# Kernel tuning notes

Hardware: AMD Instinct MI355X
Metric: run time of the kernel (lower is better)

## Reference

```python
import jax, jax.numpy as jnp
import numpy as np

HIDDEN = 1024
HEADS = 16
HEAD_DIM = HIDDEN // HEADS  # 64; softmax scale uses head_dim per SeqAttention(hidden_size=head_dim)


def setup_inputs() -> dict:
    key = jax.random.key(0)
    ks = jax.random.split(key, 7)
    B, M = 2, 2048
    s = 1.0 / np.sqrt(HIDDEN)
    return {
        "query": jax.random.normal(ks[0], (B, M, HIDDEN), jnp.float32),
        "key": jax.random.normal(ks[1], (B, M, HIDDEN), jnp.float32),
        "value": jax.random.normal(ks[2], (B, M, HIDDEN), jnp.float32),
        "Wq": jax.random.normal(ks[3], (HIDDEN, HIDDEN), jnp.float32) * s,
        "Wk": jax.random.normal(ks[4], (HIDDEN, HIDDEN), jnp.float32) * s,
        "Wv": jax.random.normal(ks[5], (HIDDEN, HIDDEN), jnp.float32) * s,
        "Wo": jax.random.normal(ks[6], (HIDDEN, HIDDEN), jnp.float32) * s,
    }


def _split_heads(x):
    # [B, T, H*D] -> [B, H, T, D]
    B, T, _ = x.shape
    return x.reshape(B, T, HEADS, HEAD_DIM).transpose(0, 2, 1, 3)


def reference(query, key, value, Wq, Wk, Wv, Wo):
    # nn.Linear(bias=False): y = x @ W.T
    q = _split_heads(query @ Wq.T)  # [B,H,M,D]
    k = _split_heads(key @ Wk.T)    # [B,H,N,D]
    v = _split_heads(value @ Wv.T)  # [B,H,N,D]
    scale = 1.0 / jnp.sqrt(jnp.asarray(HEAD_DIM, q.dtype))
    attn = jnp.einsum("bhmd,bhnd->bhmn", q, k) * scale
    attn = jax.nn.softmax(attn, axis=-1)
    out = jnp.einsum("bhmn,bhnd->bhmd", attn, v)  # [B,H,M,D]
    B, H, M, D = out.shape
    out = out.transpose(0, 2, 1, 3).reshape(B, M, H * D)
    return out @ Wo.T
```

## Files before the change

kernel.cpp:

```cpp
#include <hip/hip_runtime.h>

typedef __bf16 bf16;
typedef __bf16 bf16x2 __attribute__((ext_vector_type(2)));
typedef __bf16 bf16x8 __attribute__((ext_vector_type(8)));
typedef float  f32x4  __attribute__((ext_vector_type(4)));
typedef float  f32x16 __attribute__((ext_vector_type(16)));
typedef unsigned int u32;
typedef unsigned int u32x4 __attribute__((ext_vector_type(4)));

typedef __attribute__((address_space(1))) unsigned int gu32;
typedef __attribute__((address_space(3))) unsigned int lu32;

__device__ __forceinline__ void llds16(const void* g, void* l) {
  __builtin_amdgcn_global_load_lds((gu32*)g, (lu32*)l, 16, 0, 0);
}

__device__ __forceinline__ void cvt8(const float* __restrict__ src,
                                     bf16* __restrict__ dst, int i) {
  const float4* s4 = (const float4*)src;
  float4 a = s4[i * 2 + 0];
  float4 c = s4[i * 2 + 1];
  bf16x8 o;
  o[0] = (bf16)a.x; o[1] = (bf16)a.y; o[2] = (bf16)a.z; o[3] = (bf16)a.w;
  o[4] = (bf16)c.x; o[5] = (bf16)c.y; o[6] = (bf16)c.z; o[7] = (bf16)c.w;
  ((bf16x8*)dst)[i] = o;
}

__global__ __launch_bounds__(256) void cvt_bf16(const float* __restrict__ src,
                                                bf16* __restrict__ dst, int n8) {
  int i = blockIdx.x * blockDim.x + threadIdx.x;
  if (i < n8) cvt8(src, dst, i);
}

__global__ __launch_bounds__(256) void cvt_all(const float* __restrict__ w0,
                                               const float* __restrict__ w1,
                                               const float* __restrict__ w2,
                                               const float* __restrict__ w3,
                                               const float* __restrict__ x0,
                                               const float* __restrict__ x1,
                                               const float* __restrict__ x2,
                                               bf16* __restrict__ wdst,
                                               bf16* __restrict__ xdst) {
  const int b = blockIdx.x;
  if (b < 2048) {
    const int which = b >> 9;
    const float* src = (which == 0) ? w0 : (which == 1) ? w1 : (which == 2) ? w2 : w3;
    const int i = (b & 511) * 256 + threadIdx.x;
    cvt8(src, wdst + (size_t)which * (1u << 20), i);
  } else {
    const int b2 = b - 2048;
    const int which = b2 >> 11;
    const float* src = (which == 0) ? x0 : (which == 1) ? x1 : x2;
    const int i = (b2 & 2047) * 256 + threadIdx.x;
    cvt8(src, xdst + (size_t)which * (4u << 20), i);
  }
}

__global__ __launch_bounds__(256) void gemm_qkv(const bf16* __restrict__ A0,
                                                const bf16* __restrict__ A1,
                                                const bf16* __restrict__ A2,
                                                const bf16* __restrict__ Wb,
                                                bf16* __restrict__ qb,
                                                bf16* __restrict__ kb,
                                                bf16* __restrict__ vb,
                                                int zoff) {
  constexpr int K = 1024, BM = 128, BN = 128, BK = 32, NT = K / BK;
  __shared__ bf16 Alds[2][BM * BK];
  __shared__ bf16 Blds[2][BN * BK];
  const int t = threadIdx.x, w = t >> 6, l = t & 63;
  const int lr = l & 15, lg = l >> 4;
  const int bm = blockIdx.x * BM, bn = blockIdx.y * BN;
  const int z = blockIdx.z + zoff;
  const bf16* A = (z == 0) ? A0 : (z == 1) ? A1 : A2;
  const bf16* W = Wb + (size_t)z * (1u << 20);
  const int wm = (w >> 1) * 64, wn = (w & 1) * 64;

  f32x4 acc[4][4] = {};

  auto stage = [&](int buf, int kt) {
    const int k0 = kt * BK;
#pragma unroll
    for (int i = 0; i < 2; ++i) {
      int idx = i * 256 + t;
      int row = idx >> 2, kb2 = (idx & 3) * 16;
      llds16((const char*)A + ((size_t)(bm + row) * K + k0) * 2 + kb2,
             (char*)(&Alds[buf][0]) + (i * 4 + w) * 1024);
    }
#pragma unroll
    for (int i = 0; i < 2; ++i) {
      int idx = i * 256 + t;
      int row = idx >> 2, kb2 = (idx & 3) * 16;
      llds16((const char*)W + ((size_t)(bn + row) * K + k0) * 2 + kb2,
             (char*)(&Blds[buf][0]) + (i * 4 + w) * 1024);
    }
  };

  stage(0, 0);
  for (int kt = 0; kt < NT; ++kt) {
    __syncthreads();
    if (kt + 1 < NT) stage((kt + 1) & 1, kt + 1);
    const int cur = kt & 1;
    bf16x8 af[4], bfr[4];
#pragma unroll
    for (int i = 0; i < 4; ++i)
      af[i] = *(const bf16x8*)(&Alds[cur][(wm + i * 16 + lr) * BK + lg * 8]);
#pragma unroll
    for (int j = 0; j < 4; ++j)
      bfr[j] = *(const bf16x8*)(&Blds[cur][(wn + j * 16 + lr) * BK + lg * 8]);
    __builtin_amdgcn_s_setprio(1);
#pragma unroll
    for (int i = 0; i < 4; ++i)
#pragma unroll
      for (int j = 0; j < 4; ++j)
        acc[i][j] = __builtin_amdgcn_mfma_f32_16x16x32_bf16(af[i], bfr[j], acc[i][j], 0, 0, 0);
    __builtin_amdgcn_s_setprio(0);
  }

  bf16* Cout = (z == 0) ? qb : (z == 1) ? kb : vb;
  const float osc = (z == 0) ? 0.1803368801f : 1.0f;
#pragma unroll
  for (int i = 0; i < 4; ++i) {
#pragma unroll
    for (int j = 0; j < 4; ++j) {
#pragma unroll
      for (int r = 0; r < 4; ++r) {
        const int gm = bm + wm + i * 16 + lg * 4 + r;
        const int n  = bn + wn + j * 16 + lr;
        const int b = gm >> 11, m = gm & 2047;
        const int h = n >> 6, d = n & 63;
        const size_t off = (z < 2)
            ? ((size_t)((b * 16 + h) * 2048 + m) * 64 + d)
            : ((size_t)((b * 16 + h) * 64 + d) * 2048 + m);
        Cout[off] = (bf16)(acc[i][j][r] * osc);
      }
    }
  }
}

__global__ __launch_bounds__(256) void gemm_out(const bf16* __restrict__ A,
                                                const bf16* __restrict__ Bw,
                                                float* __restrict__ Cout) {
  constexpr int N = 1024, K = 1024;
  constexpr int BM = 128, BN = 64, BK = 32;
  __shared__ bf16 Alds[2][BM * BK];
  __shared__ bf16 Blds[2][BN * BK];
  const int t = threadIdx.x;
  const int w = t >> 6, l = t & 63;
  const int lr = l & 15, lg = l >> 4;
  const int bm = blockIdx.x * BM, bn = blockIdx.y * BN;
  const int wm = (w >> 1) * 64, wn = (w & 1) * 32;

  f32x4 acc[4][2] = {};

  auto stage = [&](int buf, int kt) {
    const int k0 = kt * BK;
#pragma unroll
    for (int i = 0; i < 2; ++i) {
      int idx = i * 256 + t;
      int row = idx >> 2, kb = (idx & 3) * 16;
      const char* g = (const char*)A + ((size_t)(bm + row) * K + k0) * 2 + kb;
      llds16(g, (char*)(&Alds[buf][0]) + (i * 4 + w) * 1024);
    }
    {
      int row = t >> 2, kb = (t & 3) * 16;
      const char* g = (const char*)Bw + ((size_t)(bn + row) * K + k0) * 2 + kb;
      llds16(g, (char*)(&Blds[buf][0]) + w * 1024);
    }
  };

  stage(0, 0);
  constexpr int NT = K / BK;
  for (int kt = 0; kt < NT; ++kt) {
    __syncthreads();
    if (kt + 1 < NT) stage((kt + 1) & 1, kt + 1);
    const int cur = kt & 1;
    bf16x8 af[4], bfr[2];
#pragma unroll
    for (int i = 0; i < 4; ++i)
      af[i] = *(const bf16x8*)(&Alds[cur][(wm + i * 16 + lr) * BK + lg * 8]);
#pragma unroll
    for (int j = 0; j < 2; ++j)
      bfr[j] = *(const bf16x8*)(&Blds[cur][(wn + j * 16 + lr) * BK + lg * 8]);
    __builtin_amdgcn_s_setprio(1);
#pragma unroll
    for (int i = 0; i < 4; ++i)
#pragma unroll
      for (int j = 0; j < 2; ++j)
        acc[i][j] = __builtin_amdgcn_mfma_f32_16x16x32_bf16(af[i], bfr[j], acc[i][j], 0, 0, 0);
    __builtin_amdgcn_s_setprio(0);
  }

#pragma unroll
  for (int i = 0; i < 4; ++i)
#pragma unroll
    for (int j = 0; j < 2; ++j)
#pragma unroll
      for (int r = 0; r < 4; ++r) {
        const int gm = bm + wm + i * 16 + lg * 4 + r;
        const int n  = bn + wn + j * 16 + lr;
        Cout[(size_t)gm * N + n] = acc[i][j][r];
      }
}

__global__ __launch_bounds__(256) void attn_fwd(const bf16* __restrict__ Qb,
                                                const bf16* __restrict__ Kb,
                                                const bf16* __restrict__ Vt,
                                                bf16* __restrict__ Out) {
  constexpr int Mlen = 2048, KVB = 64, NTT = Mlen / KVB;
  __shared__ bf16 Klds[4][KVB * 64];
  __shared__ bf16 Vlds[4][64 * KVB];
  const int t = threadIdx.x, w = t >> 6, l = t & 63;
  const int l31 = l & 31, hi = l >> 5;
  const int orig = blockIdx.x;
  const int wg = (orig & 7) * 64 + (orig >> 3);
  const int bh = wg >> 4;
  const int qr = (wg & 15) * 128 + w * 32;
  const int key = (l31 & 7) << 4;

  const bf16* qbase = Qb + ((size_t)bh * Mlen + qr + l31) * 64;
  bf16x8 qf[4];
#pragma unroll
  for (int dks = 0; dks < 4; ++dks)
    qf[dks] = *(const bf16x8*)(qbase + dks * 16 + hi * 8);

  u32x4 onesw;
  onesw[0] = 0x3F803F80u; onesw[1] = 0x3F803F80u;
  onesw[2] = 0x3F803F80u; onesw[3] = 0x3F803F80u;
  const bf16x8 ones = __builtin_bit_cast(bf16x8, onesw);

  f32x16 acco0 = {}, acco1 = {};
  f32x16 accl = {};

  const char* kTile0 = (const char*)Kb + (size_t)bh * Mlen * 64 * 2;
  const char* vBase  = (const char*)Vt + (size_t)bh * 64 * Mlen * 2;

  auto stageKV = [&](int buf, int tile) {
    const int kv0 = tile * KVB;
#pragma unroll
    for (int i = 0; i < 2; ++i) {
      int idx = i * 256 + t;
      int L = idx * 16;
      int row = L >> 7;
      int inner = (L & 127) ^ ((row & 7) << 4);
      llds16(kTile0 + (size_t)(kv0 + row) * 128 + inner,
             (char*)(&Klds[buf][0]) + (i * 4 + w) * 1024);
    }
#pragma unroll
    for (int i = 0; i < 2; ++i) {
      int idx = i * 256 + t;
      int L = idx * 16;
      int d = L >> 7;
      int inner = (L & 127) ^ ((d & 7) << 4);
      llds16(vBase + (size_t)d * (Mlen * 2) + kv0 * 2 + inner,
             (char*)(&Vlds[buf][0]) + (i * 4 + w) * 1024);
    }
  };

  auto STEP_HEAD = [&](int tile) {
    if (tile + 1 < NTT) {
      stageKV((tile + 1) & 3, tile + 1);
      asm volatile("s_waitcnt vmcnt(4)" ::: "memory");
    } else {
      asm volatile("s_waitcnt vmcnt(0)" ::: "memory");
    }
    __builtin_amdgcn_s_barrier();
    __builtin_amdgcn_sched_barrier(0);
  };
  auto QK = [&](int tile, f32x16& s0, f32x16& s1) {
    const char* kb_ = (const char*)(&Klds[tile & 3][0]);
    __builtin_amdgcn_s_setprio(1);
#pragma unroll
    for (int dks = 0; dks < 4; ++dks) {
      const int a0 = (0 * 32 + l31) * 128 + ((dks * 32 + hi * 16) ^ key);
      const int a1 = (1 * 32 + l31) * 128 + ((dks * 32 + hi * 16) ^ key);
      bf16x8 kf0 = *(const bf16x8*)(kb_ + a0);
      bf16x8 kf1 = *(const bf16x8*)(kb_ + a1);
      s0 = __builtin_amdgcn_mfma_f32_32x32x16_bf16(kf0, qf[dks], s0, 0, 0, 0);
      s1 = __builtin_amdgcn_mfma_f32_32x32x16_bf16(kf1, qf[dks], s1, 0, 0, 0);
    }
    __builtin_amdgcn_s_setprio(0);
  };
  auto EXP = [&](const f32x16& s0, const f32x16& s1, u32 (&w0)[8], u32 (&w1)[8]) {
#pragma unroll
    for (int e2 = 0; e2 < 8; ++e2) {
      const float p00 = __builtin_amdgcn_exp2f(s0[2 * e2]);
      const float p01 = __builtin_amdgcn_exp2f(s0[2 * e2 + 1]);
      const float p10 = __builtin_amdgcn_exp2f(s1[2 * e2]);
      const float p11 = __builtin_amdgcn_exp2f(s1[2 * e2 + 1]);
      bf16x2 k0; k0[0] = (bf16)p00; k0[1] = (bf16)p01;
      bf16x2 k1; k1[0] = (bf16)p10; k1[1] = (bf16)p11;
      w0[e2] = __builtin_bit_cast(u32, k0);
      w1[e2] = __builtin_bit_cast(u32, k1);
    }
  };
  auto PV = [&](int tprev, const u32 (&w0)[8], const u32 (&w1)[8]) {
    const char* vb_ = (const char*)(&Vlds[tprev & 3][0]);
    __builtin_amdgcn_s_setprio(1);
#pragma unroll
    for (int ks = 0; ks < 2; ++ks) {
      auto sa0 = __builtin_amdgcn_permlane32_swap(w0[4 * ks + 0], w0[4 * ks + 2], false, false);
      auto sa1 = __builtin_amdgcn_permlane32_swap(w0[4 * ks + 1], w0[4 * ks + 3], false, false);
      auto sb0 = __builtin_amdgcn_permlane32_swap(w1[4 * ks + 0], w1[4 * ks + 2], false, false);
      auto sb1 = __builtin_amdgcn_permlane32_swap(w1[4 * ks + 1], w1[4 * ks + 3], false, false);
      u32x4 fa, fb;
      fa[0] = (u32)sa0[0]; fa[1] = (u32)sa1[0]; fa[2] = (u32)sa0[1]; fa[3] = (u32)sa1[1];
      fb[0] = (u32)sb0[0]; fb[1] = (u32)sb1[0]; fb[2] = (u32)sb0[1]; fb[3] = (u32)sb1[1];
      const bf16x8 pa = __builtin_bit_cast(bf16x8, fa);
      const bf16x8 pb = __builtin_bit_cast(bf16x8, fb);
      const int c0 = (ks * 32 + hi * 16);
      bf16x8 va0 = *(const bf16x8*)(vb_ + (0 * 32 + l31) * 128 + ((0 * 64 + c0) ^ key));
      bf16x8 va1 = *(const bf16x8*)(vb_ + (1 * 32 + l31) * 128 + ((0 * 64 + c0) ^ key));
      bf16x8 vb0 = *(const bf16x8*)(vb_ + (0 * 32 + l31) * 128 + ((1 * 64 + c0) ^ key));
      bf16x8 vb1 = *(const bf16x8*)(vb_ + (1 * 32 + l31) * 128 + ((1 * 64 + c0) ^ key));
      acco0 = __builtin_amdgcn_mfma_f32_32x32x16_bf16(pa, va0, acco0, 0, 0, 0);
      acco1 = __builtin_amdgcn_mfma_f32_32x32x16_bf16(pa, va1, acco1, 0, 0, 0);
      accl  = __builtin_amdgcn_mfma_f32_32x32x16_bf16(pa, ones, accl, 0, 0, 0);
      acco0 = __builtin_amdgcn_mfma_f32_32x32x16_bf16(pb, vb0, acco0, 0, 0, 0);
      acco1 = __builtin_amdgcn_mfma_f32_32x32x16_bf16(pb, vb1, acco1, 0, 0, 0);
      accl  = __builtin_amdgcn_mfma_f32_32x32x16_bf16(pb, ones, accl, 0, 0, 0);
    }
    __builtin_amdgcn_s_setprio(0);
  };

  u32 wE0[8], wE1[8], wO0[8], wO1[8];
  f32x16 s0, s1;

  stageKV(0, 0);
  STEP_HEAD(0);
  s0 = f32x16{}; s1 = f32x16{};
  QK(0, s0, s1);
  EXP(s0, s1, wE0, wE1);
  for (int tp = 0; tp < 15; ++tp) {
    const int to = 2 * tp + 1;
    STEP_HEAD(to);
    s0 = f32x16{}; s1 = f32x16{};
    QK(to, s0, s1);
    PV(to - 1, wE0, wE1);
    EXP(s0, s1, wO0, wO1);
    const int te = to + 1;
    STEP_HEAD(te);
    s0 = f32x16{}; s1 = f32x16{};
    QK(te, s0, s1);
    PV(te - 1, wO0, wO1);
    EXP(s0, s1, wE0, wE1);
  }
  STEP_HEAD(31);
  s0 = f32x16{}; s1 = f32x16{};
  QK(31, s0, s1);
  PV(30, wE0, wE1);
  EXP(s0, s1, wO0, wO1);
  PV(31, wO0, wO1);

  const int b = bh >> 4, h = bh & 15;
#pragma unroll
  for (int e = 0; e < 16; ++e) {
    const int ql = (e & 3) + 8 * (e >> 2) + 4 * hi;
    const float iv = 1.0f / accl[e];
    const size_t row = (size_t)(b * 2048 + qr + ql) * 1024 + h * 64;
    Out[row + l31]      = (bf16)(acco0[e] * iv);
    Out[row + 32 + l31] = (bf16)(acco1[e] * iv);
  }
}

extern "C" void kernel_launch(void* const* d_in, const int* in_sizes, int n_in,
                              void* d_out, int out_size, void* d_ws, size_t ws_size,
                              hipStream_t stream) {
  const float* q  = (const float*)d_in[0];
  const float* k  = (const float*)d_in[1];
  const float* v  = (const float*)d_in[2];
  const float* Wq = (const float*)d_in[3];
  const float* Wk = (const float*)d_in[4];
  const float* Wv = (const float*)d_in[5];
  const float* Wo = (const float*)d_in[6];

  char* ws = (char*)d_ws;
  const dim3 cb(256);

  if (ws_size >= ((size_t)56 << 20)) {
    bf16* Wb = (bf16*)ws;
    bf16* Xq = (bf16*)(ws + (8u  << 20));
    bf16* Xk = (bf16*)(ws + (16u << 20));
    bf16* Xv = (bf16*)(ws + (24u << 20));
    bf16* qb = (bf16*)(ws + (32u << 20));
    bf16* kb = (bf16*)(ws + (40u << 20));
    bf16* vb = (bf16*)(ws + (48u << 20));
    bf16* Xa = (bf16*)(ws + (8u  << 20));

    cvt_all<<<8192, cb, 0, stream>>>(Wq, Wk, Wv, Wo, q, k, v, Wb, Xq);
    gemm_qkv<<<dim3(32, 8, 3), cb, 0, stream>>>(Xq, Xk, Xv, Wb, qb, kb, vb, 0);
    attn_fwd<<<512, cb, 0, stream>>>(qb, kb, vb, Xa);
    gemm_out<<<dim3(32, 16), cb, 0, stream>>>(Xa, Wb + 3 * (1u << 20), (float*)d_out);
  } else {
    bf16* Wb = (bf16*)ws;
    bf16* X  = (bf16*)(ws + (8u  << 20));
    bf16* qb = (bf16*)(ws + (16u << 20));
    bf16* kb = (bf16*)(ws + (24u << 20));
    bf16* vb = (bf16*)(ws + (32u << 20));
    bf16* Xa = (bf16*)(ws + (8u  << 20));

    cvt_all<<<2048, cb, 0, stream>>>(Wq, Wk, Wv, Wo, q, k, v, Wb, Wb);
    cvt_bf16<<<2048, cb, 0, stream>>>(q, X, 524288);
    gemm_qkv<<<dim3(32, 8, 1), cb, 0, stream>>>(X, X, X, Wb, qb, kb, vb, 0);
    cvt_bf16<<<2048, cb, 0, stream>>>(k, X, 524288);
    gemm_qkv<<<dim3(32, 8, 1), cb, 0, stream>>>(X, X, X, Wb, qb, kb, vb, 1);
    cvt_bf16<<<2048, cb, 0, stream>>>(v, X, 524288);
    gemm_qkv<<<dim3(32, 8, 1), cb, 0, stream>>>(X, X, X, Wb, qb, kb, vb, 2);
    attn_fwd<<<512, cb, 0, stream>>>(qb, kb, vb, Xa);
    gemm_out<<<dim3(32, 16), cb, 0, stream>>>(Xa, Wb + 3 * (1u << 20), (float*)d_out);
  }
}
```

Before: 126.0 us.

## Reorder attention pipeline so PV overlaps KV staging wait before barrier

Restructures the flash-attention main loop so that the PV matmul of the previous tile is issued right after the next K/V tile prefetch and before the vmcnt wait and barrier. The even/odd double P-register scheme is collapsed into a single P buffer because PV now consumes it before EXP overwrites it. The aim is to hide global-to-LDS load latency behind PV MFMA work instead of stalling at the barrier. In exchange, QK can no longer overlap with PV across the barrier, and the prefetch depth at startup changes to two tiles.

```diff
diff --git a/kernel.cpp b/kernel.cpp
--- a/kernel.cpp
+++ b/kernel.cpp
@@ -256,16 +256,6 @@
     }
   };
 
-  auto STEP_HEAD = [&](int tile) {
-    if (tile + 1 < NTT) {
-      stageKV((tile + 1) & 3, tile + 1);
-      asm volatile("s_waitcnt vmcnt(4)" ::: "memory");
-    } else {
-      asm volatile("s_waitcnt vmcnt(0)" ::: "memory");
-    }
-    __builtin_amdgcn_s_barrier();
-    __builtin_amdgcn_sched_barrier(0);
-  };
   auto QK = [&](int tile, f32x16& s0, f32x16& s1) {
     const char* kb_ = (const char*)(&Klds[tile & 3][0]);
     __builtin_amdgcn_s_setprio(1);
@@ -322,34 +312,37 @@
     __builtin_amdgcn_s_setprio(0);
   };
 
-  u32 wE0[8], wE1[8], wO0[8], wO1[8];
+  u32 w0[8], w1[8];
   f32x16 s0, s1;
 
   stageKV(0, 0);
-  STEP_HEAD(0);
+  stageKV(1, 1);
+  asm volatile("s_waitcnt vmcnt(4)" ::: "memory");
+  __builtin_amdgcn_s_barrier();
+  __builtin_amdgcn_sched_barrier(0);
   s0 = f32x16{}; s1 = f32x16{};
   QK(0, s0, s1);
-  EXP(s0, s1, wE0, wE1);
-  for (int tp = 0; tp < 15; ++tp) {
-    const int to = 2 * tp + 1;
-    STEP_HEAD(to);
+  EXP(s0, s1, w0, w1);
+
+  for (int tile = 1; tile < NTT - 1; ++tile) {
+    stageKV((tile + 1) & 3, tile + 1);
+    PV(tile - 1, w0, w1);
+    asm volatile("s_waitcnt vmcnt(4)" ::: "memory");
+    __builtin_amdgcn_s_barrier();
+    __builtin_amdgcn_sched_barrier(0);
     s0 = f32x16{}; s1 = f32x16{};
-    QK(to, s0, s1);
-    PV(to - 1, wE0, wE1);
-    EXP(s0, s1, wO0, wO1);
-    const int te = to + 1;
-    STEP_HEAD(te);
-    s0 = f32x16{}; s1 = f32x16{};
-    QK(te, s0, s1);
-    PV(te - 1, wO0, wO1);
-    EXP(s0, s1, wE0, wE1);
-  }
-  STEP_HEAD(31);
+    QK(tile, s0, s1);
+    EXP(s0, s1, w0, w1);
+  }
+
+  PV(30, w0, w1);
+  asm volatile("s_waitcnt vmcnt(0)" ::: "memory");
+  __builtin_amdgcn_s_barrier();
+  __builtin_amdgcn_sched_barrier(0);
   s0 = f32x16{}; s1 = f32x16{};
   QK(31, s0, s1);
-  PV(30, wE0, wE1);
-  EXP(s0, s1, wO0, wO1);
-  PV(31, wO0, wO1);
+  EXP(s0, s1, w0, w1);
+  PV(31, w0, w1);
 
   const int b = bh >> 4, h = bh & 15;
 #pragma unroll
```

Measured after the change: 127.6 us. About the same (+1.2%).
